# Optimization experiments

Hardware: AMD Instinct MI355X
Metric: run time of the kernel (lower is better)

The kernel has to match this reference:

```python
import jax, jax.numpy as jnp
import numpy as np

N, E, IN, H, G = 100000, 1600000, 64, 108, 128
N_LAYERS = 2  # hidden_dims=[108,108] -> 1 layer from hidden_dims[1:] + 1 final layer


def setup_inputs() -> dict:
    key = jax.random.key(0)
    ks = jax.random.split(key, 13)
    s = lambda fan_in: 1.0 / np.sqrt(fan_in)
    inp = {
        "nodes_feat": jax.random.normal(ks[0], (N, IN), jnp.float32),
        "edges_feat": jax.random.normal(ks[1], (E, 1), jnp.float32),
        "nodes_num_norm_sqrt": jax.random.uniform(ks[2], (N,), jnp.float32),
        "edges_num_norm_sqrt": jax.random.uniform(ks[3], (E,), jnp.float32),
        "W_emb": jax.random.uniform(ks[4], (IN, H), jnp.float32, -s(IN), s(IN)),
        "b_emb": jax.random.uniform(ks[5], (H,), jnp.float32, -s(IN), s(IN)),
        "pool_W": jax.random.uniform(ks[6], (N_LAYERS, H, H), jnp.float32, -s(H), s(H)),
        "pool_b": jax.random.uniform(ks[7], (N_LAYERS, H), jnp.float32, -s(H), s(H)),
        "app_W": jax.random.uniform(ks[8], (N_LAYERS, 2 * H, H), jnp.float32, -s(2 * H), s(2 * H)),
        "app_b": jax.random.uniform(ks[9], (N_LAYERS, H), jnp.float32, -s(2 * H), s(2 * H)),
        "src": jax.random.randint(ks[10], (E,), 0, N, jnp.int64 if jax.config.jax_enable_x64 else jnp.int32),
        "dst": jax.random.randint(ks[11], (E,), 0, N, jnp.int64 if jax.config.jax_enable_x64 else jnp.int32),
        "graph_ids": jnp.sort(jax.random.randint(ks[12], (N,), 0, G, jnp.int64 if jax.config.jax_enable_x64 else jnp.int32)),
        "n_graphs": G,
    }
    return inp


def reference(nodes_feat, edges_feat, nodes_num_norm_sqrt, edges_num_norm_sqrt,
              W_emb, b_emb, pool_W, pool_b, app_W, app_b,
              src, dst, graph_ids, n_graphs):
    n = nodes_feat.shape[0]
    # embedding_h
    h = nodes_feat @ W_emb + b_emb  # [N, H]
    # in-degree for mean aggregation (dropout = 0.0 so omitted)
    deg = jax.ops.segment_sum(jnp.ones((src.shape[0],), h.dtype), dst, num_segments=n)
    deg = jnp.maximum(deg, 1.0)[:, None]  # [N, 1]
    for i in range(pool_W.shape[0]):
        h_in = h
        # meanpool aggregator: per-message linear+ReLU == per-node transform then gather
        z = jax.nn.relu(h @ pool_W[i] + pool_b[i])  # [N, H]
        c = jax.ops.segment_sum(z[src], dst, num_segments=n) / deg  # mean over neighbors
        # NodeApply: linear(concat(h, c)) -> L2 normalize -> activation
        b = jnp.concatenate([h, c], axis=1) @ app_W[i] + app_b[i]
        b = b / jnp.maximum(jnp.linalg.norm(b, axis=1, keepdims=True), 1e-12)
        h = h_in + jax.nn.relu(b)  # residual (dims match: 108 == 108)
    # dgl.mean_nodes readout per graph
    cnt = jax.ops.segment_sum(jnp.ones((n,), h.dtype), graph_ids, num_segments=n_graphs)
    hg = jax.ops.segment_sum(h, graph_ids, num_segments=n_graphs) / jnp.maximum(cnt, 1.0)[:, None]
    return hg  # [n_graphs, H]
```

## Files before the change

### kernel.cpp

```cpp
#include <hip/hip_runtime.h>

#define HDIM 108
constexpr int G_GRAPHS = 128;
constexpr int MAXNB = 1024;
constexpr int CAP = 2560;

typedef _Float16 half8 __attribute__((ext_vector_type(8)));
typedef _Float16 half4v __attribute__((ext_vector_type(4)));
typedef float floatx4 __attribute__((ext_vector_type(4)));
typedef float floatx2 __attribute__((ext_vector_type(2)));

__device__ inline unsigned char f32_to_fp8(float t) {
#if __has_builtin(__builtin_amdgcn_cvt_pk_fp8_f32)
  return (unsigned char)(__builtin_amdgcn_cvt_pk_fp8_f32(t, t, 0, false) & 0xFF);
#else
  t = fminf(t, 448.f);
  if (t < 0.015625f) return (unsigned char)__float2int_rn(t * 512.f);
  unsigned u = __float_as_uint(t);
  unsigned lsb = (u >> 20) & 1;
  u += 0x7FFFFu + lsb;
  int e = (int)((u >> 23) & 0xFF) - 127;
  if (e > 8) return 0x7E;
  return (unsigned char)(((e + 7) << 3) | ((u >> 20) & 7));
#endif
}

template <bool HI>
__device__ inline floatx2 fp8x2_to_f32(unsigned v) {
#if __has_builtin(__builtin_amdgcn_cvt_pk_f32_fp8)
  return __builtin_amdgcn_cvt_pk_f32_fp8((int)v, HI);
#else
  unsigned b0 = HI ? ((v >> 16) & 0xFF) : (v & 0xFF);
  unsigned b1 = HI ? ((v >> 24) & 0xFF) : ((v >> 8) & 0xFF);
  floatx2 r;
  {
    unsigned s = b0 >> 7, e = (b0 >> 3) & 0xF, m = b0 & 7;
    float f = (e == 0) ? (float)m * 0.001953125f
                       : __uint_as_float(((e + 120u) << 23) | (m << 20));
    r[0] = s ? -f : f;
  }
  {
    unsigned s = b1 >> 7, e = (b1 >> 3) & 0xF, m = b1 & 7;
    float f = (e == 0) ? (float)m * 0.001953125f
                       : __uint_as_float(((e + 120u) << 23) | (m << 20));
    r[1] = s ? -f : f;
  }
  return r;
#endif
}

__global__ __launch_bounds__(1024) void k_fused0(const int* __restrict__ src, const int* __restrict__ dst,
                                                 int* __restrict__ gcur, int* __restrict__ ebuf,
                                                 const float* __restrict__ pool_W,
                                                 const float* __restrict__ app_W,
                                                 _Float16* __restrict__ wtp,
                                                 _Float16* __restrict__ wta,
                                                 const float* __restrict__ feat,
                                                 const float* __restrict__ W_emb,
                                                 const float* __restrict__ b_emb,
                                                 _Float16* __restrict__ h16,
                                                 int E, int nb, int nsc, int N) {
  __shared__ __align__(16) char smraw[29440];
  const int tid = threadIdx.x;

  if ((int)blockIdx.x < nsc) {
    int* hist = (int*)smraw;
    const int e0 = blockIdx.x * 16384;

    int gi = blockIdx.x * 1024 + tid;
    if (gi < 78848) {
      const float* srcw;
      _Float16* dstw;
      int Kpad, split, rel;
      if (gi < 14336)      { rel = gi;          srcw = pool_W;         dstw = wtp;         Kpad = 128; split = 0; }
      else if (gi < 28672) { rel = gi - 14336;  srcw = pool_W + 11664; dstw = wtp + 14336; Kpad = 128; split = 0; }
      else if (gi < 53760) { rel = gi - 28672;  srcw = app_W;          dstw = wta;         Kpad = 224; split = 1; }
      else                 { rel = gi - 53760;  srcw = app_W + 23328;  dstw = wta + 25088; Kpad = 224; split = 1; }
      int n = rel / Kpad, k = rel - n * Kpad;
      int ks;
      if (split) ks = (k < 108) ? k : (k >= 112 && k < 220) ? (k - 4) : -1;
      else       ks = (k < 108) ? k : -1;
      float v = (n < 108 && ks >= 0) ? srcw[ks * 108 + n] : 0.f;
      dstw[rel] = (_Float16)v;
    }

    for (int b = tid; b < nb; b += 1024) hist[b] = 0;
    __syncthreads();
#pragma unroll
    for (int it = 0; it < 16; it++) {
      int e = e0 + it * 1024 + tid;
      if (e < E) atomicAdd(&hist[dst[e] >> 7], 1);
    }
    __syncthreads();
    for (int b = tid; b < nb; b += 1024) {
      int h = hist[b];
      hist[b] = h ? atomicAdd(&gcur[b * 16], h) : 0;
    }
    __syncthreads();
#pragma unroll
    for (int it = 0; it < 16; it++) {
      int e = e0 + it * 1024 + tid;
      if (e < E) {
        int d = dst[e];
        int b = d >> 7;
        int rank = atomicAdd(&hist[b], 1);
        if (rank < CAP) ebuf[(size_t)b * CAP + rank] = src[e] | ((d & 127) << 20);
      }
    }
  } else {
    _Float16* As = (_Float16*)smraw;
    _Float16* Ws = (_Float16*)(smraw + 20480);
    const int sub = tid >> 8;
    const int stid = tid & 255;
    const int swave = stid >> 6;
    const int slane = stid & 63;
    const int lo = slane & 15;
    const int quad = slane >> 4;
    const int n0 = (((int)blockIdx.x - nsc) * 4 + sub) * 64;

    floatx4 acc[7];
#pragma unroll
    for (int ct = 0; ct < 7; ct++) {
      floatx4 zz = {0.f, 0.f, 0.f, 0.f};
      acc[ct] = zz;
    }

#pragma unroll 1
    for (int kc = 0; kc < 2; kc++) {
      {
        int r = stid >> 2, sg = stid & 3;
        int gn = n0 + r;
        int k = kc * 32 + sg * 8;
        half8 v = {0, 0, 0, 0, 0, 0, 0, 0};
        if (gn < N) {
          float4 f0 = *(const float4*)(feat + (size_t)gn * 64 + k);
          float4 f1 = *(const float4*)(feat + (size_t)gn * 64 + k + 4);
          v[0] = (_Float16)f0.x; v[1] = (_Float16)f0.y; v[2] = (_Float16)f0.z; v[3] = (_Float16)f0.w;
          v[4] = (_Float16)f1.x; v[5] = (_Float16)f1.y; v[6] = (_Float16)f1.z; v[7] = (_Float16)f1.w;
        }
        *(half8*)&As[sub * 2560 + r * 40 + sg * 8] = v;
      }
      if (tid < 448) {
        int nrow = tid >> 2, sg = tid & 3;
        int kb = kc * 32 + sg * 8;
        half8 v = {0, 0, 0, 0, 0, 0, 0, 0};
        if (nrow < 108) {
#pragma unroll
          for (int j = 0; j < 8; j++) v[j] = (_Float16)W_emb[(kb + j) * 108 + nrow];
        }
        *(half8*)&Ws[nrow * 40 + sg * 8] = v;
      }
      __syncthreads();

      half8 a = *(const half8*)&As[sub * 2560 + (swave * 16 + lo) * 40 + quad * 8];
#pragma unroll
      for (int ct = 0; ct < 7; ct++) {
        half8 b = *(const half8*)&Ws[(ct * 16 + lo) * 40 + quad * 8];
        acc[ct] = __builtin_amdgcn_mfma_f32_16x16x32_f16(a, b, acc[ct], 0, 0, 0);
      }
      __syncthreads();
    }

    float bias_v[7];
#pragma unroll
    for (int ct = 0; ct < 7; ct++) {
      int col = ct * 16 + lo;
      bias_v[ct] = (col < 108) ? b_emb[col] : 0.f;
    }
#pragma unroll
    for (int reg = 0; reg < 4; reg++) {
      int gr = n0 + swave * 16 + quad * 4 + reg;
      if (gr < N) {
        _Float16* op = h16 + (size_t)gr * 112 + lo;
#pragma unroll
        for (int ct = 0; ct < 7; ct++) {
          float t = acc[ct][reg] + bias_v[ct];
          op[ct * 16] = (_Float16)t;
        }
      }
    }
  }
}

__global__ __launch_bounds__(512) void k_bagg(const unsigned char* __restrict__ z, const int* __restrict__ ebuf,
                                              const int* __restrict__ gcur, _Float16* __restrict__ c16,
                                              int N, int nb) {
  __shared__ int cnts[128];
  __shared__ int scanb[128];
  __shared__ int off[129];
  __shared__ int ecur[128];
  __shared__ int esrc[CAP];
  const int tid = threadIdx.x;
  const int b = blockIdx.x;
  const int v0 = b << 7;
  int cntb = gcur[b * 16];
  if (cntb > CAP) cntb = CAP;
  const int* eb = ebuf + (size_t)b * CAP;

  if (tid < 128) cnts[tid] = 0;
  __syncthreads();
  for (int i = tid; i < cntb; i += 512) atomicAdd(&cnts[eb[i] >> 20], 1);
  __syncthreads();
  if (tid < 128) scanb[tid] = cnts[tid];
  __syncthreads();
#pragma unroll
  for (int st = 1; st < 128; st <<= 1) {
    int v = 0;
    if (tid < 128 && tid >= st) v = scanb[tid - st];
    __syncthreads();
    if (tid < 128) scanb[tid] += v;
    __syncthreads();
  }
  if (tid == 0) off[0] = 0;
  if (tid < 128) {
    off[tid + 1] = scanb[tid];
    ecur[tid] = scanb[tid] - cnts[tid];
  }
  __syncthreads();
  for (int i = tid; i < cntb; i += 512) {
    int e = eb[i];
    int p = atomicAdd(&ecur[e >> 20], 1);
    esrc[p] = e & 0xFFFFF;
  }
  __syncthreads();

  const int lane = tid & 31;
  const int grp = tid >> 5;
  if (lane >= 28) return;
  const unsigned char* __restrict__ zl = z + lane * 4;
#pragma unroll 1
  for (int r = grp; r < 128; r += 16) {
    int v = v0 + r;
    if (v >= N) continue;
    int s = off[r], e2 = off[r + 1];
    float a0 = 0.f, a1 = 0.f, a2 = 0.f, a3 = 0.f;
    int j = s;
    for (; j + 4 <= e2; j += 4) {
      unsigned q0 = *(const unsigned*)(zl + (size_t)esrc[j] * 128);
      unsigned q1 = *(const unsigned*)(zl + (size_t)esrc[j + 1] * 128);
      unsigned q2 = *(const unsigned*)(zl + (size_t)esrc[j + 2] * 128);
      unsigned q3 = *(const unsigned*)(zl + (size_t)esrc[j + 3] * 128);
      floatx2 l0 = fp8x2_to_f32<false>(q0), h0 = fp8x2_to_f32<true>(q0);
      floatx2 l1 = fp8x2_to_f32<false>(q1), h1 = fp8x2_to_f32<true>(q1);
      floatx2 l2 = fp8x2_to_f32<false>(q2), h2 = fp8x2_to_f32<true>(q2);
      floatx2 l3 = fp8x2_to_f32<false>(q3), h3 = fp8x2_to_f32<true>(q3);
      a0 += (l0[0] + l1[0]) + (l2[0] + l3[0]);
      a1 += (l0[1] + l1[1]) + (l2[1] + l3[1]);
      a2 += (h0[0] + h1[0]) + (h2[0] + h3[0]);
      a3 += (h0[1] + h1[1]) + (h2[1] + h3[1]);
    }
    for (; j < e2; j++) {
      unsigned q0 = *(const unsigned*)(zl + (size_t)esrc[j] * 128);
      floatx2 l0 = fp8x2_to_f32<false>(q0), h0 = fp8x2_to_f32<true>(q0);
      a0 += l0[0]; a1 += l0[1]; a2 += h0[0]; a3 += h0[1];
    }
    int d = e2 - s;
    float inv = 1.f / (float)(d > 0 ? d : 1);
    half4v r4;
    r4[0] = (_Float16)(a0 * inv); r4[1] = (_Float16)(a1 * inv);
    r4[2] = (_Float16)(a2 * inv); r4[3] = (_Float16)(a3 * inv);
    *(half4v*)(c16 + (size_t)v * 112 + lane * 4) = r4;
  }
}

template <int KCH, int MODE>
__global__ __launch_bounds__(256) void k_mmf(const void* Asrc, const _Float16* __restrict__ c16,
                                             const _Float16* __restrict__ Wt, const float* __restrict__ bias,
                                             void* outp, int N) {
  constexpr int KW = KCH * 32;
  __shared__ _Float16 As[2][64 * 40];
  __shared__ _Float16 Ws[2][112 * 40];

  const int tid = threadIdx.x;
  const int wave = tid >> 6;
  const int lane = tid & 63;
  const int lo = lane & 15;
  const int quad = lane >> 4;
  const int n0 = blockIdx.x * 64;
  const _Float16* h16 = (const _Float16*)Asrc;

  const int ar = tid >> 2, asg = tid & 3;
  const int gnA = n0 + ar;
  const int wrow0 = tid >> 2, wsg0 = tid & 3;
  const int widx1 = tid + 256;
  const int wrow1 = widx1 >> 2, wsg1 = widx1 & 3;

  auto loadA = [&](int kc) -> half8 {
    int k = kc * 32 + asg * 8;
    half8 v = {0, 0, 0, 0, 0, 0, 0, 0};
    if (gnA < N) {
      if (MODE == 2) {
        const _Float16* sp = (k < 112) ? (h16 + (size_t)gnA * 112 + k)
                                       : (c16 + (size_t)gnA * 112 + (k - 112));
        v = *(const half8*)sp;
      } else {
        if (k < 112) v = *(const half8*)(h16 + (size_t)gnA * 112 + k);
      }
    }
    return v;
  };

  half8 aR = loadA(0);
  half8 wR0 = *(const half8*)(Wt + (size_t)wrow0 * KW + wsg0 * 8);
  half8 wR1 = {0, 0, 0, 0, 0, 0, 0, 0};
  if (tid < 192) wR1 = *(const half8*)(Wt + (size_t)wrow1 * KW + wsg1 * 8);

  *(half8*)&As[0][ar * 40 + asg * 8] = aR;
  *(half8*)&Ws[0][wrow0 * 40 + wsg0 * 8] = wR0;
  if (tid < 192) *(half8*)&Ws[0][wrow1 * 40 + wsg1 * 8] = wR1;
  __syncthreads();

  floatx4 acc[7];
#pragma unroll
  for (int ct = 0; ct < 7; ct++) {
    floatx4 zz = {0.f, 0.f, 0.f, 0.f};
    acc[ct] = zz;
  }

#pragma unroll 1
  for (int kc = 0; kc < KCH; kc++) {
    const int cur = kc & 1, nxt = cur ^ 1;
    if (kc + 1 < KCH) {
      aR = loadA(kc + 1);
      wR0 = *(const half8*)(Wt + (size_t)wrow0 * KW + (kc + 1) * 32 + wsg0 * 8);
      if (tid < 192) wR1 = *(const half8*)(Wt + (size_t)wrow1 * KW + (kc + 1) * 32 + wsg1 * 8);
    }

    half8 a = *(const half8*)&As[cur][(wave * 16 + lo) * 40 + quad * 8];
#pragma unroll
    for (int ct = 0; ct < 7; ct++) {
      half8 b = *(const half8*)&Ws[cur][(ct * 16 + lo) * 40 + quad * 8];
      acc[ct] = __builtin_amdgcn_mfma_f32_16x16x32_f16(a, b, acc[ct], 0, 0, 0);
    }

    if (kc + 1 < KCH) {
      *(half8*)&As[nxt][ar * 40 + asg * 8] = aR;
      *(half8*)&Ws[nxt][wrow0 * 40 + wsg0 * 8] = wR0;
      if (tid < 192) *(half8*)&Ws[nxt][wrow1 * 40 + wsg1 * 8] = wR1;
      __syncthreads();
    }
  }

  float bias_v[7];
#pragma unroll
  for (int ct = 0; ct < 7; ct++) {
    int col = ct * 16 + lo;
    bias_v[ct] = (col < 108) ? bias[col] : 0.f;
  }

  if (MODE == 2) {
    _Float16* out16 = (_Float16*)outp;
#pragma unroll
    for (int reg = 0; reg < 4; reg++) {
      int gr = n0 + wave * 16 + quad * 4 + reg;
      float bv[7];
      float ssq = 0.f;
#pragma unroll
      for (int ct = 0; ct < 7; ct++) {
        float t = acc[ct][reg] + bias_v[ct];
        bv[ct] = t;
        ssq += t * t;
      }
#pragma unroll
      for (int s = 1; s < 16; s <<= 1) ssq += __shfl_xor(ssq, s, 16);
      float scale = 1.f / fmaxf(sqrtf(ssq), 1e-12f);
      if (gr < N) {
        _Float16* hp = out16 + (size_t)gr * 112 + lo;
#pragma unroll
        for (int ct = 0; ct < 7; ct++) {
          float hv = (float)hp[ct * 16];
          hp[ct * 16] = (_Float16)(hv + fmaxf(bv[ct] * scale, 0.f));
        }
      }
    }
  } else {
    unsigned char* outb = (unsigned char*)outp;
#pragma unroll
    for (int reg = 0; reg < 4; reg++) {
      int gr = n0 + wave * 16 + quad * 4 + reg;
      if (gr < N) {
        unsigned char* op = outb + (size_t)gr * 128 + lo;
#pragma unroll
        for (int ct = 0; ct < 7; ct++) {
          float t = fmaxf(acc[ct][reg] + bias_v[ct], 0.f);
          op[ct * 16] = f32_to_fp8(t);
        }
      }
    }
  }
}

__global__ __launch_bounds__(256) void k_readout(const _Float16* __restrict__ h, const int* __restrict__ gid,
                                                 float* __restrict__ hg, int N) {
  const int CH = 16;
  const int lane = threadIdx.x & 31;
  const int grp = threadIdx.x >> 5;
  int start = (blockIdx.x * 8 + grp) * CH;
  if (start >= N || lane >= 27) return;
  int end = min(start + CH, N);
  float a0 = 0.f, a1 = 0.f, a2 = 0.f, a3 = 0.f;
  int cur = gid[start];
  for (int i = start; i < end; i++) {
    int g = gid[i];
    if (g != cur) {
      float* base = &hg[(size_t)cur * HDIM + lane * 4];
      atomicAdd(base + 0, a0); atomicAdd(base + 1, a1);
      atomicAdd(base + 2, a2); atomicAdd(base + 3, a3);
      a0 = a1 = a2 = a3 = 0.f;
      cur = g;
    }
    half4v v = *(const half4v*)(h + (size_t)i * 112 + lane * 4);
    a0 += (float)v[0]; a1 += (float)v[1]; a2 += (float)v[2]; a3 += (float)v[3];
  }
  float* base = &hg[(size_t)cur * HDIM + lane * 4];
  atomicAdd(base + 0, a0); atomicAdd(base + 1, a1);
  atomicAdd(base + 2, a2); atomicAdd(base + 3, a3);
}

__global__ __launch_bounds__(256) void k_div(const float* __restrict__ hg, const int* __restrict__ gid,
                                             float* __restrict__ out, int total, int N) {
  int i = blockIdx.x * 256 + threadIdx.x;
  if (i < total) {
    int g = i / HDIM;
    int lo = 0, hi = N;
    while (lo < hi) { int m = (lo + hi) >> 1; if (gid[m] < g) lo = m + 1; else hi = m; }
    int lb = lo;
    lo = 0; hi = N;
    while (lo < hi) { int m = (lo + hi) >> 1; if (gid[m] <= g) lo = m + 1; else hi = m; }
    int c = lo - lb;
    out[i] = hg[i] / (float)(c > 0 ? c : 1);
  }
}

extern "C" void kernel_launch(void* const* d_in, const int* in_sizes, int n_in,
                              void* d_out, int out_size, void* d_ws, size_t ws_size,
                              hipStream_t stream) {
  (void)n_in; (void)ws_size; (void)out_size;
  const float* nodes_feat = (const float*)d_in[0];
  const float* W_emb = (const float*)d_in[4];
  const float* b_emb = (const float*)d_in[5];
  const float* pool_W = (const float*)d_in[6];
  const float* pool_b = (const float*)d_in[7];
  const float* app_W = (const float*)d_in[8];
  const float* app_b = (const float*)d_in[9];
  const int* src = (const int*)d_in[10];
  const int* dst = (const int*)d_in[11];
  const int* gid = (const int*)d_in[12];
  const int N = in_sizes[2];
  const int E = in_sizes[10];
  float* out = (float*)d_out;

  const int nb = (N + 127) >> 7;
  const int nbMM = (N + 63) / 64;
  const int nsc = (E + 16383) / 16384;
  const int ngb = (nbMM + 3) / 4;

  char* ws = (char*)d_ws;
  size_t off = 0;
  auto alloc = [&](size_t bytes) -> size_t {
    size_t o = off;
    off += (bytes + 1023) & ~size_t(1023);
    return o;
  };
  size_t o_gcur = alloc((size_t)MAXNB * 16 * 4);
  size_t o_hg   = alloc((size_t)G_GRAPHS * HDIM * 4);
  size_t zero_bytes = off;
  size_t o_ebuf = alloc((size_t)MAXNB * CAP * 4);
  size_t o_h  = alloc((size_t)N * 112 * 2);
  size_t o_z  = alloc((size_t)N * 128);
  size_t o_c  = alloc((size_t)N * 112 * 2);
  size_t o_wp = alloc((size_t)2 * 112 * 128 * 2);
  size_t o_wa = alloc((size_t)2 * 112 * 224 * 2);

  int*           gcur = (int*)(ws + o_gcur);
  float*         hg   = (float*)(ws + o_hg);
  int*           ebuf = (int*)(ws + o_ebuf);
  _Float16*      h16  = (_Float16*)(ws + o_h);
  unsigned char* z8   = (unsigned char*)(ws + o_z);
  _Float16*      c16  = (_Float16*)(ws + o_c);
  _Float16*      wtp  = (_Float16*)(ws + o_wp);
  _Float16*      wta  = (_Float16*)(ws + o_wa);

  (void)hipMemsetAsync(d_ws, 0, zero_bytes, stream);

  k_fused0<<<nsc + ngb, 1024, 0, stream>>>(src, dst, gcur, ebuf,
                                           pool_W, app_W, wtp, wta,
                                           nodes_feat, W_emb, b_emb, h16,
                                           E, nb, nsc, N);

  for (int i = 0; i < 2; i++) {
    k_mmf<4, 1><<<nbMM, 256, 0, stream>>>(h16, nullptr, wtp + i * 14336,
                                          pool_b + i * HDIM, z8, N);
    k_bagg<<<nb, 512, 0, stream>>>(z8, ebuf, gcur, c16, N, nb);
    k_mmf<7, 2><<<nbMM, 256, 0, stream>>>(h16, c16, wta + i * 25088,
                                          app_b + i * HDIM, h16, N);
  }

  k_readout<<<(N + 8 * 16 - 1) / (8 * 16), 256, 0, stream>>>(h16, gid, hg, N);
  k_div<<<(G_GRAPHS * HDIM + 255) / 256, 256, 0, stream>>>(hg, gid, out, G_GRAPHS * HDIM, N);
}
```

Baseline: 312.1 us.

## Fuse graph readout into final apply GEMM and enlarge edge-scatter chunks

The final layer's apply GEMM gains a MODE 3 epilogue. It writes the residual-updated rows into shared memory and accumulates per-graph sums with atomics, which removes the separate readout kernel and the final h16 write and reread. The edge-bucketing part of the fused setup kernel now gives each block three times as many edges and loops over the weight conversion. This cuts the block count and the global atomics on bucket counters, but reduces parallelism in that phase.

```diff
diff --git a/kernel.cpp b/kernel.cpp
--- a/kernel.cpp
+++ b/kernel.cpp
@@ -65,10 +65,9 @@
 
   if ((int)blockIdx.x < nsc) {
     int* hist = (int*)smraw;
-    const int e0 = blockIdx.x * 16384;
-
-    int gi = blockIdx.x * 1024 + tid;
-    if (gi < 78848) {
+    const int e0 = blockIdx.x * 49152;
+
+    for (int gi = blockIdx.x * 1024 + tid; gi < 78848; gi += nsc * 1024) {
       const float* srcw;
       _Float16* dstw;
       int Kpad, split, rel;
@@ -86,8 +85,8 @@
 
     for (int b = tid; b < nb; b += 1024) hist[b] = 0;
     __syncthreads();
-#pragma unroll
-    for (int it = 0; it < 16; it++) {
+#pragma unroll 1
+    for (int it = 0; it < 48; it++) {
       int e = e0 + it * 1024 + tid;
       if (e < E) atomicAdd(&hist[dst[e] >> 7], 1);
     }
@@ -97,8 +96,8 @@
       hist[b] = h ? atomicAdd(&gcur[b * 16], h) : 0;
     }
     __syncthreads();
-#pragma unroll
-    for (int it = 0; it < 16; it++) {
+#pragma unroll 1
+    for (int it = 0; it < 48; it++) {
       int e = e0 + it * 1024 + tid;
       if (e < E) {
         int d = dst[e];
@@ -266,10 +265,10 @@
 template <int KCH, int MODE>
 __global__ __launch_bounds__(256) void k_mmf(const void* Asrc, const _Float16* __restrict__ c16,
                                              const _Float16* __restrict__ Wt, const float* __restrict__ bias,
-                                             void* outp, int N) {
+                                             void* outp, const int* __restrict__ gid,
+                                             float* __restrict__ hg, int N) {
   constexpr int KW = KCH * 32;
-  __shared__ _Float16 As[2][64 * 40];
-  __shared__ _Float16 Ws[2][112 * 40];
+  __shared__ _Float16 smem[14080];
 
   const int tid = threadIdx.x;
   const int wave = tid >> 6;
@@ -289,7 +288,7 @@
     int k = kc * 32 + asg * 8;
     half8 v = {0, 0, 0, 0, 0, 0, 0, 0};
     if (gnA < N) {
-      if (MODE == 2) {
+      if (MODE >= 2) {
         const _Float16* sp = (k < 112) ? (h16 + (size_t)gnA * 112 + k)
                                        : (c16 + (size_t)gnA * 112 + (k - 112));
         v = *(const half8*)sp;
@@ -305,9 +304,9 @@
   half8 wR1 = {0, 0, 0, 0, 0, 0, 0, 0};
   if (tid < 192) wR1 = *(const half8*)(Wt + (size_t)wrow1 * KW + wsg1 * 8);
 
-  *(half8*)&As[0][ar * 40 + asg * 8] = aR;
-  *(half8*)&Ws[0][wrow0 * 40 + wsg0 * 8] = wR0;
-  if (tid < 192) *(half8*)&Ws[0][wrow1 * 40 + wsg1 * 8] = wR1;
+  *(half8*)&smem[ar * 40 + asg * 8] = aR;
+  *(half8*)&smem[5120 + wrow0 * 40 + wsg0 * 8] = wR0;
+  if (tid < 192) *(half8*)&smem[5120 + wrow1 * 40 + wsg1 * 8] = wR1;
   __syncthreads();
 
   floatx4 acc[7];
@@ -326,17 +325,17 @@
       if (tid < 192) wR1 = *(const half8*)(Wt + (size_t)wrow1 * KW + (kc + 1) * 32 + wsg1 * 8);
     }
 
-    half8 a = *(const half8*)&As[cur][(wave * 16 + lo) * 40 + quad * 8];
+    half8 a = *(const half8*)&smem[cur * 2560 + (wave * 16 + lo) * 40 + quad * 8];
 #pragma unroll
     for (int ct = 0; ct < 7; ct++) {
-      half8 b = *(const half8*)&Ws[cur][(ct * 16 + lo) * 40 + quad * 8];
+      half8 b = *(const half8*)&smem[5120 + cur * 4480 + (ct * 16 + lo) * 40 + quad * 8];
       acc[ct] = __builtin_amdgcn_mfma_f32_16x16x32_f16(a, b, acc[ct], 0, 0, 0);
     }
 
     if (kc + 1 < KCH) {
-      *(half8*)&As[nxt][ar * 40 + asg * 8] = aR;
-      *(half8*)&Ws[nxt][wrow0 * 40 + wsg0 * 8] = wR0;
-      if (tid < 192) *(half8*)&Ws[nxt][wrow1 * 40 + wsg1 * 8] = wR1;
+      *(half8*)&smem[nxt * 2560 + ar * 40 + asg * 8] = aR;
+      *(half8*)&smem[5120 + nxt * 4480 + wrow0 * 40 + wsg0 * 8] = wR0;
+      if (tid < 192) *(half8*)&smem[5120 + nxt * 4480 + wrow1 * 40 + wsg1 * 8] = wR1;
       __syncthreads();
     }
   }
@@ -348,11 +347,13 @@
     bias_v[ct] = (col < 108) ? bias[col] : 0.f;
   }
 
-  if (MODE == 2) {
+  if (MODE >= 2) {
     _Float16* out16 = (_Float16*)outp;
+    if (MODE == 3) __syncthreads();
 #pragma unroll
     for (int reg = 0; reg < 4; reg++) {
-      int gr = n0 + wave * 16 + quad * 4 + reg;
+      int rl = wave * 16 + quad * 4 + reg;
+      int gr = n0 + rl;
       float bv[7];
       float ssq = 0.f;
 #pragma unroll
@@ -365,12 +366,40 @@
       for (int s = 1; s < 16; s <<= 1) ssq += __shfl_xor(ssq, s, 16);
       float scale = 1.f / fmaxf(sqrtf(ssq), 1e-12f);
       if (gr < N) {
-        _Float16* hp = out16 + (size_t)gr * 112 + lo;
 #pragma unroll
         for (int ct = 0; ct < 7; ct++) {
-          float hv = (float)hp[ct * 16];
-          hp[ct * 16] = (_Float16)(hv + fmaxf(bv[ct] * scale, 0.f));
+          float hv = (float)h16[(size_t)gr * 112 + ct * 16 + lo];
+          float t = hv + fmaxf(bv[ct] * scale, 0.f);
+          if (MODE == 2) out16[(size_t)gr * 112 + ct * 16 + lo] = (_Float16)t;
+          else           smem[rl * 120 + ct * 16 + lo] = (_Float16)t;
         }
+      }
+    }
+    if (MODE == 3) {
+      __syncthreads();
+      const int lane31 = tid & 31;
+      const int grp8 = tid >> 5;
+      int r0 = grp8 * 8;
+      if (lane31 < 27 && n0 + r0 < N) {
+        float a0 = 0.f, a1 = 0.f, a2 = 0.f, a3 = 0.f;
+        int cur = gid[n0 + r0];
+        for (int r = r0; r < r0 + 8; r++) {
+          int gn = n0 + r;
+          if (gn >= N) break;
+          int g = gid[gn];
+          if (g != cur) {
+            float* base = &hg[(size_t)cur * HDIM + lane31 * 4];
+            atomicAdd(base + 0, a0); atomicAdd(base + 1, a1);
+            atomicAdd(base + 2, a2); atomicAdd(base + 3, a3);
+            a0 = a1 = a2 = a3 = 0.f;
+            cur = g;
+          }
+          half4v v = *(const half4v*)&smem[r * 120 + lane31 * 4];
+          a0 += (float)v[0]; a1 += (float)v[1]; a2 += (float)v[2]; a3 += (float)v[3];
+        }
+        float* base = &hg[(size_t)cur * HDIM + lane31 * 4];
+        atomicAdd(base + 0, a0); atomicAdd(base + 1, a1);
+        atomicAdd(base + 2, a2); atomicAdd(base + 3, a3);
       }
     }
   } else {
@@ -388,33 +417,6 @@
       }
     }
   }
-}
-
-__global__ __launch_bounds__(256) void k_readout(const _Float16* __restrict__ h, const int* __restrict__ gid,
-                                                 float* __restrict__ hg, int N) {
-  const int CH = 16;
-  const int lane = threadIdx.x & 31;
-  const int grp = threadIdx.x >> 5;
-  int start = (blockIdx.x * 8 + grp) * CH;
-  if (start >= N || lane >= 27) return;
-  int end = min(start + CH, N);
-  float a0 = 0.f, a1 = 0.f, a2 = 0.f, a3 = 0.f;
-  int cur = gid[start];
-  for (int i = start; i < end; i++) {
-    int g = gid[i];
-    if (g != cur) {
-      float* base = &hg[(size_t)cur * HDIM + lane * 4];
-      atomicAdd(base + 0, a0); atomicAdd(base + 1, a1);
-      atomicAdd(base + 2, a2); atomicAdd(base + 3, a3);
-      a0 = a1 = a2 = a3 = 0.f;
-      cur = g;
-    }
-    half4v v = *(const half4v*)(h + (size_t)i * 112 + lane * 4);
-    a0 += (float)v[0]; a1 += (float)v[1]; a2 += (float)v[2]; a3 += (float)v[3];
-  }
-  float* base = &hg[(size_t)cur * HDIM + lane * 4];
-  atomicAdd(base + 0, a0); atomicAdd(base + 1, a1);
-  atomicAdd(base + 2, a2); atomicAdd(base + 3, a3);
 }
 
 __global__ __launch_bounds__(256) void k_div(const float* __restrict__ hg, const int* __restrict__ gid,
@@ -452,7 +454,7 @@
 
   const int nb = (N + 127) >> 7;
   const int nbMM = (N + 63) / 64;
-  const int nsc = (E + 16383) / 16384;
+  const int nsc = (E + 49151) / 49152;
   const int ngb = (nbMM + 3) / 4;
 
   char* ws = (char*)d_ws;
@@ -488,14 +490,12 @@
                                            nodes_feat, W_emb, b_emb, h16,
                                            E, nb, nsc, N);
 
-  for (int i = 0; i < 2; i++) {
-    k_mmf<4, 1><<<nbMM, 256, 0, stream>>>(h16, nullptr, wtp + i * 14336,
-                                          pool_b + i * HDIM, z8, N);
-    k_bagg<<<nb, 512, 0, stream>>>(z8, ebuf, gcur, c16, N, nb);
-    k_mmf<7, 2><<<nbMM, 256, 0, stream>>>(h16, c16, wta + i * 25088,
-                                          app_b + i * HDIM, h16, N);
-  }
-
-  k_readout<<<(N + 8 * 16 - 1) / (8 * 16), 256, 0, stream>>>(h16, gid, hg, N);
+  k_mmf<4, 1><<<nbMM, 256, 0, stream>>>(h16, nullptr, wtp, pool_b, z8, nullptr, nullptr, N);
+  k_bagg<<<nb, 512, 0, stream>>>(z8, ebuf, gcur, c16, N, nb);
+  k_mmf<7, 2><<<nbMM, 256, 0, stream>>>(h16, c16, wta, app_b, h16, nullptr, nullptr, N);
+  k_mmf<4, 1><<<nbMM, 256, 0, stream>>>(h16, nullptr, wtp + 14336, pool_b + HDIM, z8, nullptr, nullptr, N);
+  k_bagg<<<nb, 512, 0, stream>>>(z8, ebuf, gcur, c16, N, nb);
+  k_mmf<7, 3><<<nbMM, 256, 0, stream>>>(h16, c16, wta + 25088, app_b + HDIM, nullptr, gid, hg, N);
+
   k_div<<<(G_GRAPHS * HDIM + 255) / 256, 256, 0, stream>>>(hg, gid, out, G_GRAPHS * HDIM, N);
 }
```

Result: slower. 406.6 us (+30.3%).

## Fuse graph readout and division into one per-graph block reduction kernel

Applied to the files above, without the earlier changes.

The atomic-based readout kernel and the separate division kernel are replaced by a single kernel that launches one 1024-thread block per graph. Each block binary-searches the sorted graph ids for its node range, reduces node features through shared memory, and writes the mean directly. This drops a launch, the float atomics and the zero-initialised accumulator buffer. The trade-off is only 128 blocks, each scanning about 780 rows, which may leave much of the GPU idle. Separately, the matmul kernel's shared arrays are merged into one flat buffer with manual offsets, which does not change its behaviour.

```diff
diff --git a/kernel.cpp b/kernel.cpp
--- a/kernel.cpp
+++ b/kernel.cpp
@@ -268,8 +268,7 @@
                                              const _Float16* __restrict__ Wt, const float* __restrict__ bias,
                                              void* outp, int N) {
   constexpr int KW = KCH * 32;
-  __shared__ _Float16 As[2][64 * 40];
-  __shared__ _Float16 Ws[2][112 * 40];
+  __shared__ _Float16 smem[14080];
 
   const int tid = threadIdx.x;
   const int wave = tid >> 6;
@@ -305,9 +304,9 @@
   half8 wR1 = {0, 0, 0, 0, 0, 0, 0, 0};
   if (tid < 192) wR1 = *(const half8*)(Wt + (size_t)wrow1 * KW + wsg1 * 8);
 
-  *(half8*)&As[0][ar * 40 + asg * 8] = aR;
-  *(half8*)&Ws[0][wrow0 * 40 + wsg0 * 8] = wR0;
-  if (tid < 192) *(half8*)&Ws[0][wrow1 * 40 + wsg1 * 8] = wR1;
+  *(half8*)&smem[ar * 40 + asg * 8] = aR;
+  *(half8*)&smem[5120 + wrow0 * 40 + wsg0 * 8] = wR0;
+  if (tid < 192) *(half8*)&smem[5120 + wrow1 * 40 + wsg1 * 8] = wR1;
   __syncthreads();
 
   floatx4 acc[7];
@@ -326,17 +325,17 @@
       if (tid < 192) wR1 = *(const half8*)(Wt + (size_t)wrow1 * KW + (kc + 1) * 32 + wsg1 * 8);
     }
 
-    half8 a = *(const half8*)&As[cur][(wave * 16 + lo) * 40 + quad * 8];
+    half8 a = *(const half8*)&smem[cur * 2560 + (wave * 16 + lo) * 40 + quad * 8];
 #pragma unroll
     for (int ct = 0; ct < 7; ct++) {
-      half8 b = *(const half8*)&Ws[cur][(ct * 16 + lo) * 40 + quad * 8];
+      half8 b = *(const half8*)&smem[5120 + cur * 4480 + (ct * 16 + lo) * 40 + quad * 8];
       acc[ct] = __builtin_amdgcn_mfma_f32_16x16x32_f16(a, b, acc[ct], 0, 0, 0);
     }
 
     if (kc + 1 < KCH) {
-      *(half8*)&As[nxt][ar * 40 + asg * 8] = aR;
-      *(half8*)&Ws[nxt][wrow0 * 40 + wsg0 * 8] = wR0;
-      if (tid < 192) *(half8*)&Ws[nxt][wrow1 * 40 + wsg1 * 8] = wR1;
+      *(half8*)&smem[nxt * 2560 + ar * 40 + asg * 8] = aR;
+      *(half8*)&smem[5120 + nxt * 4480 + wrow0 * 40 + wsg0 * 8] = wR0;
+      if (tid < 192) *(half8*)&smem[5120 + nxt * 4480 + wrow1 * 40 + wsg1 * 8] = wR1;
       __syncthreads();
     }
   }
@@ -390,45 +389,36 @@
   }
 }
 
-__global__ __launch_bounds__(256) void k_readout(const _Float16* __restrict__ h, const int* __restrict__ gid,
-                                                 float* __restrict__ hg, int N) {
-  const int CH = 16;
-  const int lane = threadIdx.x & 31;
-  const int grp = threadIdx.x >> 5;
-  int start = (blockIdx.x * 8 + grp) * CH;
-  if (start >= N || lane >= 27) return;
-  int end = min(start + CH, N);
+__global__ __launch_bounds__(1024) void k_rdout(const _Float16* __restrict__ h, const int* __restrict__ gid,
+                                                float* __restrict__ out, int N) {
+  __shared__ float part[32][116];
+  const int g = blockIdx.x;
+  int lo = 0, hi = N;
+  while (lo < hi) { int m = (lo + hi) >> 1; if (gid[m] < g) lo = m + 1; else hi = m; }
+  const int lb = lo;
+  lo = 0; hi = N;
+  while (lo < hi) { int m = (lo + hi) >> 1; if (gid[m] <= g) lo = m + 1; else hi = m; }
+  const int ub = lo;
+  const int cnt = ub - lb;
+
+  const int tid = threadIdx.x;
+  const int lane = tid & 31;
+  const int grp = tid >> 5;
   float a0 = 0.f, a1 = 0.f, a2 = 0.f, a3 = 0.f;
-  int cur = gid[start];
-  for (int i = start; i < end; i++) {
-    int g = gid[i];
-    if (g != cur) {
-      float* base = &hg[(size_t)cur * HDIM + lane * 4];
-      atomicAdd(base + 0, a0); atomicAdd(base + 1, a1);
-      atomicAdd(base + 2, a2); atomicAdd(base + 3, a3);
-      a0 = a1 = a2 = a3 = 0.f;
-      cur = g;
-    }
-    half4v v = *(const half4v*)(h + (size_t)i * 112 + lane * 4);
-    a0 += (float)v[0]; a1 += (float)v[1]; a2 += (float)v[2]; a3 += (float)v[3];
-  }
-  float* base = &hg[(size_t)cur * HDIM + lane * 4];
-  atomicAdd(base + 0, a0); atomicAdd(base + 1, a1);
-  atomicAdd(base + 2, a2); atomicAdd(base + 3, a3);
-}
-
-__global__ __launch_bounds__(256) void k_div(const float* __restrict__ hg, const int* __restrict__ gid,
-                                             float* __restrict__ out, int total, int N) {
-  int i = blockIdx.x * 256 + threadIdx.x;
-  if (i < total) {
-    int g = i / HDIM;
-    int lo = 0, hi = N;
-    while (lo < hi) { int m = (lo + hi) >> 1; if (gid[m] < g) lo = m + 1; else hi = m; }
-    int lb = lo;
-    lo = 0; hi = N;
-    while (lo < hi) { int m = (lo + hi) >> 1; if (gid[m] <= g) lo = m + 1; else hi = m; }
-    int c = lo - lb;
-    out[i] = hg[i] / (float)(c > 0 ? c : 1);
+  if (lane < 28) {
+    for (int i = lb + grp; i < ub; i += 32) {
+      half4v v = *(const half4v*)(h + (size_t)i * 112 + lane * 4);
+      a0 += (float)v[0]; a1 += (float)v[1]; a2 += (float)v[2]; a3 += (float)v[3];
+    }
+    float4 p; p.x = a0; p.y = a1; p.z = a2; p.w = a3;
+    *(float4*)&part[grp][lane * 4] = p;
+  }
+  __syncthreads();
+  if (tid < 112) {
+    float s = 0.f;
+#pragma unroll
+    for (int k = 0; k < 32; k++) s += part[k][tid];
+    if (tid < 108) out[(size_t)g * HDIM + tid] = s / (float)(cnt > 0 ? cnt : 1);
   }
 }
 
@@ -463,7 +453,6 @@
     return o;
   };
   size_t o_gcur = alloc((size_t)MAXNB * 16 * 4);
-  size_t o_hg   = alloc((size_t)G_GRAPHS * HDIM * 4);
   size_t zero_bytes = off;
   size_t o_ebuf = alloc((size_t)MAXNB * CAP * 4);
   size_t o_h  = alloc((size_t)N * 112 * 2);
@@ -473,7 +462,6 @@
   size_t o_wa = alloc((size_t)2 * 112 * 224 * 2);
 
   int*           gcur = (int*)(ws + o_gcur);
-  float*         hg   = (float*)(ws + o_hg);
   int*           ebuf = (int*)(ws + o_ebuf);
   _Float16*      h16  = (_Float16*)(ws + o_h);
   unsigned char* z8   = (unsigned char*)(ws + o_z);
@@ -496,6 +484,5 @@
                                           app_b + i * HDIM, h16, N);
   }
 
-  k_readout<<<(N + 8 * 16 - 1) / (8 * 16), 256, 0, stream>>>(h16, gid, hg, N);
-  k_div<<<(G_GRAPHS * HDIM + 255) / 256, 256, 0, stream>>>(hg, gid, out, G_GRAPHS * HDIM, N);
-}
+  k_rdout<<<G_GRAPHS, 1024, 0, stream>>>(h16, gid, out, N);
+}
```

Result: faster. 293.3 us (-6.0%).
